# Optimization experiments

Measured on AMD Instinct MI355X. Metric: run time of the kernel, lower is better.

Reference implementation:

```python
import jax, jax.numpy as jnp
import numpy as np

T = 16777216            # flat replay-buffer length (timesteps)
DISCOUNT = 0.99         # gamma
FINAL_REWARD = 0.0      # bootstrap value for the last timestep
TERM_PROB = 0.001       # ~1000-step episodes


def setup_inputs() -> dict:
    key = jax.random.key(0)
    k1, k2 = jax.random.split(key)
    reward = jax.random.normal(k1, (T,), dtype=jnp.float32)
    terminal = jax.random.bernoulli(k2, TERM_PROB, (T,))
    return {"terminal": terminal, "reward": reward}


def _discounted_cumret(terminal, reward):
    # Reverse-time linear recurrence (same math as tf.scan over reversed seq):
    #   c_t = r_t                      if terminal_t
    #   c_t = r_t + discount * c_{t+1} otherwise
    # i.e. c_t = a_t * c_{t+1} + b_t with a_t = discount*(1-term_t), b_t = r_t.
    # Expressed as a (log-depth) associative scan over the reversed sequence.
    a = jnp.where(terminal, jnp.zeros((), reward.dtype),
                  jnp.asarray(DISCOUNT, reward.dtype))
    a_rev = a[::-1]
    b_rev = reward[::-1]
    # fold the initializer (final_reward) into the first reversed element
    b_rev = b_rev.at[0].add(a_rev[0] * jnp.asarray(FINAL_REWARD, reward.dtype))

    def combine(e1, e2):
        # composition of affine maps x -> a*x + b (e1 applied first)
        a1, b1 = e1
        a2, b2 = e2
        return a1 * a2, a2 * b1 + b2

    _, y_rev = jax.lax.associative_scan(combine, (a_rev, b_rev))
    return y_rev[::-1]


def reference(terminal, reward):
    return _discounted_cumret(terminal, reward)
```

## Files before the change

### kernel.cpp

```cpp
#include <hip/hip_runtime.h>


constexpr int   TPB   = 1024;
constexpr int   NWAV  = TPB / 64;
constexpr int   IPTC  = 8;
constexpr int   TILE  = TPB * IPTC;
constexpr float DISC  = 0.99f;
constexpr float L2DISC = -0.0144995696f;

constexpr int   FTPB  = 256;

__device__ __forceinline__ void wave_suffix_scan(float& A, float& B, int lane) {
    #pragma unroll
    for (int off = 1; off < 64; off <<= 1) {
        float oA = __shfl_down(A, off, 64);
        float oB = __shfl_down(B, off, 64);
        if (lane + off < 64) { B = A * oB + B; A = A * oA; }
    }
}

__global__ __launch_bounds__(TPB) void k_local(
        const int* __restrict__ term, const float* __restrict__ rew,
        float* __restrict__ out, float2* __restrict__ agg,
        int* __restrict__ lastT, long long T) {
    __shared__ float2 sWA[NWAV];
    __shared__ int    sLast[NWAV];

    const int t = threadIdx.x;
    const int lane = t & 63, wav = t >> 6;
    const int b = blockIdx.x;
    const long long lo = (long long)b * TILE;
    const bool fastblk = (lo + TILE <= T);

    float At, Bt;
    int   lt;

    if (fastblk) {
        const long long base = lo + (long long)t * IPTC;

        float4 bR[IPTC / 4];
        int4   bT[IPTC / 4];
        {
            const float4* rp = (const float4*)(rew + base);
            const int4*   tp = (const int4*)(term + base);
            #pragma unroll
            for (int q = 0; q < IPTC / 4; ++q) {
                bR[q] = rp[q];
                bT[q] = tp[q];
            }
        }

        float r[IPTC];
        unsigned mask = 0;
        #pragma unroll
        for (int q = 0; q < IPTC / 4; ++q) {
            float4 rv = bR[q];
            int4   tv = bT[q];
            r[4*q+0] = rv.x; r[4*q+1] = rv.y; r[4*q+2] = rv.z; r[4*q+3] = rv.w;
            mask |= (tv.x ? 1u : 0u) << (4*q+0);
            mask |= (tv.y ? 1u : 0u) << (4*q+1);
            mask |= (tv.z ? 1u : 0u) << (4*q+2);
            mask |= (tv.w ? 1u : 0u) << (4*q+3);
        }

        float A = 1.f, B = 0.f;
        #pragma unroll
        for (int k = IPTC - 1; k >= 0; --k) {
            float ak = ((mask >> k) & 1u) ? 0.f : DISC;
            B = ak * B + r[k]; A = ak * A;
        }

        float IA = A, IB = B;
        wave_suffix_scan(IA, IB, lane);

        int myLast = mask ? (int)(base + (31 - __clz(mask))) : -1;
        #pragma unroll
        for (int off = 32; off > 0; off >>= 1)
            myLast = max(myLast, __shfl_down(myLast, off, 64));

        if (lane == 0) { sWA[wav] = make_float2(IA, IB); sLast[wav] = myLast; }
        __syncthreads();

        float2 g = sWA[0];
        int cl = sLast[0];
        #pragma unroll
        for (int w = 1; w < NWAV; ++w) {
            float2 h = sWA[w];
            g.y = g.x * h.y + g.y; g.x = g.x * h.x;
            cl = max(cl, sLast[w]);
        }
        float EWA = 1.f, EWB = 0.f;
        #pragma unroll
        for (int w = 0; w < NWAV; ++w)
            if (w > wav) { float2 h = sWA[w]; EWB = EWA*h.y + EWB; EWA = EWA*h.x; }

        float EA = __shfl_down(IA, 1, 64);
        float EB = __shfl_down(IB, 1, 64);
        if (lane == 63) { EA = 1.f; EB = 0.f; }

        float y = EA * EWB + EB;

        #pragma unroll
        for (int k = IPTC - 1; k >= 0; --k) {
            float ak = ((mask >> k) & 1u) ? 0.f : DISC;
            y = ak * y + r[k]; r[k] = y;
        }

        float4* op = (float4*)(out + base);
        #pragma unroll
        for (int q = 0; q < IPTC / 4; ++q)
            op[q] = make_float4(r[4*q+0], r[4*q+1], r[4*q+2], r[4*q+3]);

        At = g.x; Bt = g.y; lt = cl;
    } else {
        const long long base = lo + (long long)t * IPTC;
        float r[IPTC];
        unsigned mask = 0;
        #pragma unroll
        for (int k = 0; k < IPTC; ++k) {
            long long i = base + k;
            if (i < T) { r[k] = rew[i]; mask |= (term[i] ? 1u : 0u) << k; }
            else       { r[k] = 0.f; }
        }
        float A = 1.f, B = 0.f;
        #pragma unroll
        for (int k = IPTC - 1; k >= 0; --k) {
            float ak = ((mask >> k) & 1u) ? 0.f : DISC;
            if (base + k >= T) ak = 1.f;
            B = ak * B + r[k]; A = ak * A;
        }
        float IA = A, IB = B;
        wave_suffix_scan(IA, IB, lane);

        int myLast = mask ? (int)(base + (31 - __clz(mask))) : -1;
        #pragma unroll
        for (int off = 32; off > 0; off >>= 1)
            myLast = max(myLast, __shfl_down(myLast, off, 64));

        if (lane == 0) { sWA[wav] = make_float2(IA, IB); sLast[wav] = myLast; }
        __syncthreads();

        float2 g = sWA[0];
        int cl = sLast[0];
        #pragma unroll
        for (int w = 1; w < NWAV; ++w) {
            float2 h = sWA[w];
            g.y = g.x * h.y + g.y; g.x = g.x * h.x;
            cl = max(cl, sLast[w]);
        }
        float EWA = 1.f, EWB = 0.f;
        #pragma unroll
        for (int w = 0; w < NWAV; ++w)
            if (w > wav) { float2 h = sWA[w]; EWB = EWA*h.y + EWB; EWA = EWA*h.x; }

        float EA = __shfl_down(IA, 1, 64);
        float EB = __shfl_down(IB, 1, 64);
        if (lane == 63) { EA = 1.f; EB = 0.f; }

        float y = EA * EWB + EB;

        #pragma unroll
        for (int k = IPTC - 1; k >= 0; --k) {
            float ak = ((mask >> k) & 1u) ? 0.f : DISC;
            if (base + k >= T) ak = 1.f;
            y = ak * y + r[k]; r[k] = y;
        }
        #pragma unroll
        for (int k = 0; k < IPTC; ++k) {
            long long i = base + k;
            if (i < T) out[i] = r[k];
        }

        At = g.x; Bt = g.y; lt = cl;
    }

    if (t == 0) {
        agg[b] = make_float2(At, Bt);
        lastT[b] = max(lt, (int)lo - 1);
    }
}

__global__ __launch_bounds__(FTPB) void k_fix(
        const float2* __restrict__ agg, const int* __restrict__ lastT,
        float* __restrict__ out, int numBlocks, long long T) {
    __shared__ float2 sWB[FTPB / 64];

    const int t = threadIdx.x;
    const int lane = t & 63, wav = t >> 6;
    const int b = blockIdx.x;

    const int cpt = (numBlocks + FTPB - 1) / FTPB;
    float VA = 1.f, VB = 0.f;
    #pragma unroll
    for (int k = cpt - 1; k >= 0; --k) {
        int g = t * cpt + k;
        if (g > b && g < numBlocks) {
            float2 q = agg[g];
            VB = q.x * VB + q.y; VA = q.x * VA;
        }
    }
    wave_suffix_scan(VA, VB, lane);
    if (lane == 0) sWB[wav] = make_float2(VA, VB);
    __syncthreads();

    float FA = sWB[0].x, FB = sWB[0].y;
    #pragma unroll
    for (int w = 1; w < FTPB / 64; ++w) {
        float2 h = sWB[w];
        FB = FA * h.y + FB; FA = FA * h.x;
    }
    const float yin = FB;
    if (yin == 0.f) return;

    const long long lo = (long long)b * TILE;
    const long long hi = min(lo + (long long)TILE, T) - 1;
    const long long start = (long long)lastT[b] + 1;

    for (long long i = start + t; i <= hi; i += FTPB) {
        float d = (float)(int)(hi + 1 - i);
        out[i] += exp2f(d * L2DISC) * yin;
    }
}

extern "C" void kernel_launch(void* const* d_in, const int* in_sizes, int n_in,
                              void* d_out, int out_size, void* d_ws, size_t ws_size,
                              hipStream_t stream) {
    const int*   term = (const int*)d_in[0];
    const float* rew  = (const float*)d_in[1];
    float*       out  = (float*)d_out;

    const long long T = (long long)in_sizes[1];
    const int numBlocks = (int)((T + TILE - 1) / TILE);

    float2* agg   = (float2*)d_ws;
    int*    lastT = (int*)(agg + numBlocks);

    k_local<<<numBlocks, TPB, 0, stream>>>(term, rew, out, agg, lastT, T);
    k_fix  <<<numBlocks, FTPB, 0, stream>>>(agg, lastT, out, numBlocks, T);
}
```

Baseline: 176.8 us.

## Make each wavefront own a 4096-element segment and drop block-level sync

```diff
diff --git a/kernel.cpp b/kernel.cpp
--- a/kernel.cpp
+++ b/kernel.cpp
@@ -1,14 +1,13 @@
 #include <hip/hip_runtime.h>
 
 
-constexpr int   TPB   = 1024;
-constexpr int   NWAV  = TPB / 64;
-constexpr int   IPTC  = 8;
-constexpr int   TILE  = TPB * IPTC;
-constexpr float DISC  = 0.99f;
+constexpr int   SEG    = 4096;
+constexpr int   IPL    = SEG / 64;
+constexpr int   TPB    = 256;
+constexpr int   WPB    = TPB / 64;
+constexpr int   FTPB   = 256;
+constexpr float DISC   = 0.99f;
 constexpr float L2DISC = -0.0144995696f;
-
-constexpr int   FTPB  = 256;
 
 __device__ __forceinline__ void wave_suffix_scan(float& A, float& B, int lane) {
     #pragma unroll
@@ -22,179 +21,118 @@
 __global__ __launch_bounds__(TPB) void k_local(
         const int* __restrict__ term, const float* __restrict__ rew,
         float* __restrict__ out, float2* __restrict__ agg,
-        int* __restrict__ lastT, long long T) {
-    __shared__ float2 sWA[NWAV];
-    __shared__ int    sLast[NWAV];
+        int* __restrict__ lastT, int nSeg, long long T) {
+    const int lane = threadIdx.x & 63;
+    const int wav  = threadIdx.x >> 6;
+    const int seg  = blockIdx.x * WPB + wav;
+    if (seg >= nSeg) return;
 
-    const int t = threadIdx.x;
-    const int lane = t & 63, wav = t >> 6;
-    const int b = blockIdx.x;
-    const long long lo = (long long)b * TILE;
-    const bool fastblk = (lo + TILE <= T);
+    const long long segLo = (long long)seg * SEG;
+    const long long base  = segLo + (long long)lane * IPL;
+    const bool fast = (segLo + SEG <= T);
 
-    float At, Bt;
-    int   lt;
+    float r[IPL];
+    unsigned long long mask = 0;
 
-    if (fastblk) {
-        const long long base = lo + (long long)t * IPTC;
+    if (fast) {
+        const float4* rp = (const float4*)(rew + base);
+        const int4*   tp = (const int4*)(term + base);
+        #pragma unroll
+        for (int q = 0; q < IPL / 4; ++q) {
+            float4 rv = rp[q];
+            int4   tv = tp[q];
+            r[4*q+0] = rv.x; r[4*q+1] = rv.y; r[4*q+2] = rv.z; r[4*q+3] = rv.w;
+            unsigned mb = (tv.x ? 1u : 0u) | (tv.y ? 2u : 0u)
+                        | (tv.z ? 4u : 0u) | (tv.w ? 8u : 0u);
+            mask |= (unsigned long long)mb << (4*q);
+        }
+    } else {
+        #pragma unroll 4
+        for (int k = 0; k < IPL; ++k) {
+            long long i = base + k;
+            if (i < T) { r[k] = rew[i]; if (term[i]) mask |= 1ull << k; }
+            else       { r[k] = 0.f; }
+        }
+    }
 
-        float4 bR[IPTC / 4];
-        int4   bT[IPTC / 4];
-        {
-            const float4* rp = (const float4*)(rew + base);
-            const int4*   tp = (const int4*)(term + base);
-            #pragma unroll
-            for (int q = 0; q < IPTC / 4; ++q) {
-                bR[q] = rp[q];
-                bT[q] = tp[q];
-            }
-        }
-
-        float r[IPTC];
-        unsigned mask = 0;
+    float A = 1.f, B = 0.f;
+    if (fast) {
         #pragma unroll
-        for (int q = 0; q < IPTC / 4; ++q) {
-            float4 rv = bR[q];
-            int4   tv = bT[q];
-            r[4*q+0] = rv.x; r[4*q+1] = rv.y; r[4*q+2] = rv.z; r[4*q+3] = rv.w;
-            mask |= (tv.x ? 1u : 0u) << (4*q+0);
-            mask |= (tv.y ? 1u : 0u) << (4*q+1);
-            mask |= (tv.z ? 1u : 0u) << (4*q+2);
-            mask |= (tv.w ? 1u : 0u) << (4*q+3);
-        }
-
-        float A = 1.f, B = 0.f;
-        #pragma unroll
-        for (int k = IPTC - 1; k >= 0; --k) {
-            float ak = ((mask >> k) & 1u) ? 0.f : DISC;
+        for (int k = IPL - 1; k >= 0; --k) {
+            float ak = ((mask >> k) & 1ull) ? 0.f : DISC;
             B = ak * B + r[k]; A = ak * A;
         }
-
-        float IA = A, IB = B;
-        wave_suffix_scan(IA, IB, lane);
-
-        int myLast = mask ? (int)(base + (31 - __clz(mask))) : -1;
-        #pragma unroll
-        for (int off = 32; off > 0; off >>= 1)
-            myLast = max(myLast, __shfl_down(myLast, off, 64));
-
-        if (lane == 0) { sWA[wav] = make_float2(IA, IB); sLast[wav] = myLast; }
-        __syncthreads();
-
-        float2 g = sWA[0];
-        int cl = sLast[0];
-        #pragma unroll
-        for (int w = 1; w < NWAV; ++w) {
-            float2 h = sWA[w];
-            g.y = g.x * h.y + g.y; g.x = g.x * h.x;
-            cl = max(cl, sLast[w]);
-        }
-        float EWA = 1.f, EWB = 0.f;
-        #pragma unroll
-        for (int w = 0; w < NWAV; ++w)
-            if (w > wav) { float2 h = sWA[w]; EWB = EWA*h.y + EWB; EWA = EWA*h.x; }
-
-        float EA = __shfl_down(IA, 1, 64);
-        float EB = __shfl_down(IB, 1, 64);
-        if (lane == 63) { EA = 1.f; EB = 0.f; }
-
-        float y = EA * EWB + EB;
-
-        #pragma unroll
-        for (int k = IPTC - 1; k >= 0; --k) {
-            float ak = ((mask >> k) & 1u) ? 0.f : DISC;
-            y = ak * y + r[k]; r[k] = y;
-        }
-
-        float4* op = (float4*)(out + base);
-        #pragma unroll
-        for (int q = 0; q < IPTC / 4; ++q)
-            op[q] = make_float4(r[4*q+0], r[4*q+1], r[4*q+2], r[4*q+3]);
-
-        At = g.x; Bt = g.y; lt = cl;
     } else {
-        const long long base = lo + (long long)t * IPTC;
-        float r[IPTC];
-        unsigned mask = 0;
-        #pragma unroll
-        for (int k = 0; k < IPTC; ++k) {
-            long long i = base + k;
-            if (i < T) { r[k] = rew[i]; mask |= (term[i] ? 1u : 0u) << k; }
-            else       { r[k] = 0.f; }
-        }
-        float A = 1.f, B = 0.f;
-        #pragma unroll
-        for (int k = IPTC - 1; k >= 0; --k) {
-            float ak = ((mask >> k) & 1u) ? 0.f : DISC;
+        #pragma unroll 4
+        for (int k = IPL - 1; k >= 0; --k) {
+            float ak = ((mask >> k) & 1ull) ? 0.f : DISC;
             if (base + k >= T) ak = 1.f;
             B = ak * B + r[k]; A = ak * A;
         }
-        float IA = A, IB = B;
-        wave_suffix_scan(IA, IB, lane);
+    }
 
-        int myLast = mask ? (int)(base + (31 - __clz(mask))) : -1;
+    float IA = A, IB = B;
+    wave_suffix_scan(IA, IB, lane);
+
+    long long myLast = mask ? (base + (63 - __clzll(mask))) : -1;
+    #pragma unroll
+    for (int off = 32; off > 0; off >>= 1) {
+        long long o = __shfl_down(myLast, off, 64);
+        myLast = max(myLast, o);
+    }
+
+    float EA = __shfl_down(IA, 1, 64);
+    float EB = __shfl_down(IB, 1, 64);
+    if (lane == 63) { EA = 1.f; EB = 0.f; }
+    (void)EA;
+
+    float y = EB;
+    if (fast) {
         #pragma unroll
-        for (int off = 32; off > 0; off >>= 1)
-            myLast = max(myLast, __shfl_down(myLast, off, 64));
-
-        if (lane == 0) { sWA[wav] = make_float2(IA, IB); sLast[wav] = myLast; }
-        __syncthreads();
-
-        float2 g = sWA[0];
-        int cl = sLast[0];
+        for (int k = IPL - 1; k >= 0; --k) {
+            float ak = ((mask >> k) & 1ull) ? 0.f : DISC;
+            y = ak * y + r[k]; r[k] = y;
+        }
+        float4* op = (float4*)(out + base);
         #pragma unroll
-        for (int w = 1; w < NWAV; ++w) {
-            float2 h = sWA[w];
-            g.y = g.x * h.y + g.y; g.x = g.x * h.x;
-            cl = max(cl, sLast[w]);
-        }
-        float EWA = 1.f, EWB = 0.f;
-        #pragma unroll
-        for (int w = 0; w < NWAV; ++w)
-            if (w > wav) { float2 h = sWA[w]; EWB = EWA*h.y + EWB; EWA = EWA*h.x; }
-
-        float EA = __shfl_down(IA, 1, 64);
-        float EB = __shfl_down(IB, 1, 64);
-        if (lane == 63) { EA = 1.f; EB = 0.f; }
-
-        float y = EA * EWB + EB;
-
-        #pragma unroll
-        for (int k = IPTC - 1; k >= 0; --k) {
-            float ak = ((mask >> k) & 1u) ? 0.f : DISC;
+        for (int q = 0; q < IPL / 4; ++q)
+            op[q] = make_float4(r[4*q+0], r[4*q+1], r[4*q+2], r[4*q+3]);
+    } else {
+        #pragma unroll 4
+        for (int k = IPL - 1; k >= 0; --k) {
+            float ak = ((mask >> k) & 1ull) ? 0.f : DISC;
             if (base + k >= T) ak = 1.f;
             y = ak * y + r[k]; r[k] = y;
         }
-        #pragma unroll
-        for (int k = 0; k < IPTC; ++k) {
+        for (int k = 0; k < IPL; ++k) {
             long long i = base + k;
             if (i < T) out[i] = r[k];
         }
-
-        At = g.x; Bt = g.y; lt = cl;
     }
 
-    if (t == 0) {
-        agg[b] = make_float2(At, Bt);
-        lastT[b] = max(lt, (int)lo - 1);
+    if (lane == 0) {
+        agg[seg]   = make_float2(IA, IB);
+        lastT[seg] = (int)max(myLast, segLo - 1);
     }
 }
 
 __global__ __launch_bounds__(FTPB) void k_fix(
         const float2* __restrict__ agg, const int* __restrict__ lastT,
-        float* __restrict__ out, int numBlocks, long long T) {
+        float* __restrict__ out, int nSeg, long long T) {
     __shared__ float2 sWB[FTPB / 64];
 
     const int t = threadIdx.x;
     const int lane = t & 63, wav = t >> 6;
     const int b = blockIdx.x;
+    const int s0 = 2 * b;
+    const int s1 = 2 * b + 1;
 
-    const int cpt = (numBlocks + FTPB - 1) / FTPB;
+    const int cpt = (nSeg + FTPB - 1) / FTPB;
     float VA = 1.f, VB = 0.f;
     #pragma unroll
     for (int k = cpt - 1; k >= 0; --k) {
         int g = t * cpt + k;
-        if (g > b && g < numBlocks) {
+        if (g > s1 && g < nSeg) {
             float2 q = agg[g];
             VB = q.x * VB + q.y; VA = q.x * VA;
         }
@@ -209,16 +147,33 @@
         float2 h = sWB[w];
         FB = FA * h.y + FB; FA = FA * h.x;
     }
-    const float yin = FB;
-    if (yin == 0.f) return;
 
-    const long long lo = (long long)b * TILE;
-    const long long hi = min(lo + (long long)TILE, T) - 1;
-    const long long start = (long long)lastT[b] + 1;
+    const float yin1 = FB;
+    float yin0;
+    if (s1 < nSeg) {
+        float2 a1 = agg[s1];
+        yin0 = a1.x * yin1 + a1.y;
+    } else {
+        yin0 = yin1;
+    }
 
-    for (long long i = start + t; i <= hi; i += FTPB) {
-        float d = (float)(int)(hi + 1 - i);
-        out[i] += exp2f(d * L2DISC) * yin;
+    if (s1 < nSeg && yin1 != 0.f) {
+        const long long sLo = (long long)s1 * SEG;
+        const long long sHi = min(sLo + (long long)SEG, T) - 1;
+        const long long start = (long long)lastT[s1] + 1;
+        for (long long i = start + t; i <= sHi; i += FTPB) {
+            float d = (float)(int)(sHi + 1 - i);
+            out[i] += exp2f(d * L2DISC) * yin1;
+        }
+    }
+    if (s0 < nSeg && yin0 != 0.f) {
+        const long long sLo = (long long)s0 * SEG;
+        const long long sHi = min(sLo + (long long)SEG, T) - 1;
+        const long long start = (long long)lastT[s0] + 1;
+        for (long long i = start + t; i <= sHi; i += FTPB) {
+            float d = (float)(int)(sHi + 1 - i);
+            out[i] += exp2f(d * L2DISC) * yin0;
+        }
     }
 }
 
@@ -230,11 +185,14 @@
     float*       out  = (float*)d_out;
 
     const long long T = (long long)in_sizes[1];
-    const int numBlocks = (int)((T + TILE - 1) / TILE);
+    const int nSeg = (int)((T + SEG - 1) / SEG);
 
     float2* agg   = (float2*)d_ws;
-    int*    lastT = (int*)(agg + numBlocks);
+    int*    lastT = (int*)(agg + nSeg);
 
-    k_local<<<numBlocks, TPB, 0, stream>>>(term, rew, out, agg, lastT, T);
-    k_fix  <<<numBlocks, FTPB, 0, stream>>>(agg, lastT, out, numBlocks, T);
+    const int blocksLocal = (nSeg + WPB - 1) / WPB;
+    const int blocksFix   = (nSeg + 1) / 2;
+
+    k_local<<<blocksLocal, TPB, 0, stream>>>(term, rew, out, agg, lastT, nSeg, T);
+    k_fix  <<<blocksFix,   FTPB, 0, stream>>>(agg, lastT, out, nSeg, T);
 }
```

After: 258.6 us. 46.3% more time.
